# Kernel tuning notes

Hardware: AMD Instinct MI355X
Metric: run time of the kernel (lower is better)

## Reference

```python
import jax, jax.numpy as jnp
import numpy as np

SPARSITY = 0.5  # cur_sparsity set during training; 0.0 default would make masking a no-op
WEIGHT_BETA = 1.0
MASK_ALPHA1 = 1.0
MASK_ALPHA2 = 1.0


def binarize(mask_scores, sparsity):
    # SparseBinarizer.forward: prune (set to 0) the `num_prune` smallest scores globally.
    num_prune = int(mask_scores.size * sparsity)  # static: sparsity is a Python float
    flat = mask_scores.reshape(-1)
    prune_idx = jnp.argsort(flat)[:num_prune]
    mask = jnp.ones_like(flat).at[prune_idx].set(0.0)
    return mask.reshape(mask_scores.shape)


def setup_inputs() -> dict:
    key = jax.random.key(0)
    ks = jax.random.split(key, 9)
    out_f, in_f, r = 4096, 4096, 8
    tokens = 8192  # batch 4 * seq 2048
    return {
        "x": jax.random.normal(ks[0], (tokens, in_f), dtype=jnp.float32),
        "weight": jax.random.normal(ks[1], (out_f, in_f), dtype=jnp.float32) * 0.02,
        "bias": jax.random.normal(ks[2], (out_f,), dtype=jnp.float32) * 0.02,
        "weight_U": jax.random.normal(ks[3], (out_f, r), dtype=jnp.float32),
        "weight_V": jnp.zeros((r, in_f), dtype=jnp.float32),
        "mask_scores_A": jax.random.normal(ks[4], (out_f, r), dtype=jnp.float32),
        "mask_scores_B": jnp.zeros((r, in_f), dtype=jnp.float32),
        "mask_scores_R": jnp.zeros((out_f,), dtype=jnp.float32),
        "mask_scores_C": jnp.zeros((in_f,), dtype=jnp.float32),
    }


def reference(x, weight, bias, weight_U, weight_V, mask_scores_A, mask_scores_B,
              mask_scores_R, mask_scores_C):
    # weight = W + beta * U @ V   (low-rank weight reconstruction)
    w = weight + WEIGHT_BETA * (weight_U @ weight_V)
    # mask_scores = |w| + a1 * A @ B + a2 * (R[:,None] + C[None,:])
    mask_scores = (jnp.abs(w)
                   + MASK_ALPHA1 * (mask_scores_A @ mask_scores_B)
                   + MASK_ALPHA2 * (mask_scores_R[:, None] + mask_scores_C[None, :]))
    mask = binarize(mask_scores, SPARSITY)
    masked_weight = mask * w  # [out_f, in_f]
    # nn.Linear: x @ W^T + b
    return x @ masked_weight.T + bias
```

## Files before the change

kernel.cpp:

```cpp
#include <hip/hip_runtime.h>
#include <stdint.h>

#define TOKENS 8192
#define OUT_F  4096
#define IN_F   4096
#define RNK    8
#define KPRUNE 8388608u
#define CAP3   16384u

typedef unsigned short u16;
typedef float  f32x4  __attribute__((ext_vector_type(4)));
typedef short  bf16x8 __attribute__((ext_vector_type(8)));
typedef unsigned short u16x4 __attribute__((ext_vector_type(4)));
typedef unsigned short u16x8 __attribute__((ext_vector_type(8)));

#define XB_OFF    0ull
#define WB_OFF    67108864ull
#define CTL_OFF   100663296ull
#define H1_OFF    0
#define H2_OFF    16384
#define CNT3_OFF  32768
#define LIST3_OFF 32772
#define CTL_ZERO_U32 8193

__device__ __forceinline__ u16 f2bf(float f) {
    uint32_t u = __float_as_uint(f);
    u += 0x7fffu + ((u >> 16) & 1u);
    return (u16)(u >> 16);
}

__device__ __forceinline__ uint32_t fkey(float s) {
    uint32_t u = __float_as_uint(s);
    return (u & 0x80000000u) ? ~u : (u | 0x80000000u);
}

__device__ __forceinline__ void hsel(const uint32_t* __restrict__ hist, uint32_t k,
                                     volatile uint32_t* scr,
                                     uint32_t& bin, uint32_t& below)
{
    const int t = threadIdx.x;
    const int lane = t & 63, w = t >> 6;
    uint32_t v[16]; uint32_t s = 0;
#pragma unroll
    for (int j = 0; j < 16; ++j) { v[j] = hist[t*16 + j]; s += v[j]; }
    uint32_t sc = s;
#pragma unroll
    for (int d = 1; d < 64; d <<= 1) {
        uint32_t o = __shfl_up(sc, d, 64);
        if (lane >= d) sc += o;
    }
    if (lane == 63) scr[w] = sc;
    __syncthreads();
    uint32_t woff = 0;
    for (int ww = 0; ww < w; ++ww) woff += scr[ww];
    const uint32_t pre = woff + sc - s;
    if (pre < k && pre + s >= k) {
        uint32_t bb = pre;
#pragma unroll
        for (int j = 0; j < 16; ++j) {
            if (bb < k && bb + v[j] >= k) { scr[4] = (uint32_t)(t*16 + j); scr[5] = bb; }
            bb += v[j];
        }
    }
    __syncthreads();
    bin = scr[4]; below = scr[5];
    __syncthreads();
}

struct S2 { float4 w0, w1; uint4 k0, k1; };
__device__ __forceinline__ S2 score2(const float* __restrict__ W,
                                     const float* __restrict__ V,
                                     const float* __restrict__ B,
                                     const float* __restrict__ C,
                                     const float* uu0, const float* uu1,
                                     const float* aa0, const float* aa1,
                                     float ro0, float ro1, int o0, int i)
{
    const float4 cc = *(const float4*)&C[i];
    float4 w0 = *(const float4*)&W[(size_t)o0*IN_F + i];
    float4 w1 = *(const float4*)&W[(size_t)(o0+1)*IN_F + i];
#pragma unroll
    for (int r = 0; r < RNK; ++r) {
        const float4 v4 = *(const float4*)&V[r*IN_F + i];
        const float a0 = uu0[r], a1 = uu1[r];
        w0.x = fmaf(a0, v4.x, w0.x); w0.y = fmaf(a0, v4.y, w0.y);
        w0.z = fmaf(a0, v4.z, w0.z); w0.w = fmaf(a0, v4.w, w0.w);
        w1.x = fmaf(a1, v4.x, w1.x); w1.y = fmaf(a1, v4.y, w1.y);
        w1.z = fmaf(a1, v4.z, w1.z); w1.w = fmaf(a1, v4.w, w1.w);
    }
    float4 s0, s1;
    s0.x = fabsf(w0.x); s0.y = fabsf(w0.y); s0.z = fabsf(w0.z); s0.w = fabsf(w0.w);
    s1.x = fabsf(w1.x); s1.y = fabsf(w1.y); s1.z = fabsf(w1.z); s1.w = fabsf(w1.w);
#pragma unroll
    for (int r = 0; r < RNK; ++r) {
        const float4 b4 = *(const float4*)&B[r*IN_F + i];
        const float a0 = aa0[r], a1 = aa1[r];
        s0.x = fmaf(a0, b4.x, s0.x); s0.y = fmaf(a0, b4.y, s0.y);
        s0.z = fmaf(a0, b4.z, s0.z); s0.w = fmaf(a0, b4.w, s0.w);
        s1.x = fmaf(a1, b4.x, s1.x); s1.y = fmaf(a1, b4.y, s1.y);
        s1.z = fmaf(a1, b4.z, s1.z); s1.w = fmaf(a1, b4.w, s1.w);
    }
    s0.x += ro0 + cc.x; s0.y += ro0 + cc.y; s0.z += ro0 + cc.z; s0.w += ro0 + cc.w;
    s1.x += ro1 + cc.x; s1.y += ro1 + cc.y; s1.z += ro1 + cc.z; s1.w += ro1 + cc.w;
    S2 o;
    o.w0 = w0; o.w1 = w1;
    o.k0.x = fkey(s0.x); o.k0.y = fkey(s0.y); o.k0.z = fkey(s0.z); o.k0.w = fkey(s0.w);
    o.k1.x = fkey(s1.x); o.k1.y = fkey(s1.y); o.k1.z = fkey(s1.z); o.k1.w = fkey(s1.w);
    return o;
}

#define LOAD_ROWPARAMS                                                        \
    float uu0[RNK], uu1[RNK], aa0[RNK], aa1[RNK];                             \
    _Pragma("unroll") for (int r = 0; r < RNK; ++r) {                         \
        uu0[r] = U[o0*RNK + r];   uu1[r] = U[(o0+1)*RNK + r];                 \
        aa0[r] = A[o0*RNK + r];   aa1[r] = A[(o0+1)*RNK + r];                 \
    }                                                                         \
    const float ro0 = R[o0], ro1 = R[o0 + 1];

__global__ void convx_kernel(const float* __restrict__ x, u16* __restrict__ xB,
                             uint32_t* __restrict__ ctl)
{
    const int t = threadIdx.x;
    if (blockIdx.x < 33) {
        const int i = blockIdx.x * 256 + t;
        if (i < CTL_ZERO_U32) ctl[i] = 0u;
    }
    const size_t idx = (size_t)blockIdx.x * 256 + t;
    const float4* xv = (const float4*)x;
    float4 a = xv[idx*2];
    float4 b = xv[idx*2 + 1];
    u16x8 o;
    o[0]=f2bf(a.x); o[1]=f2bf(a.y); o[2]=f2bf(a.z); o[3]=f2bf(a.w);
    o[4]=f2bf(b.x); o[5]=f2bf(b.y); o[6]=f2bf(b.z); o[7]=f2bf(b.w);
    *((u16x8*)xB + idx) = o;
}

__global__ void prep_kernel(const float* __restrict__ W, const float* __restrict__ U,
                            const float* __restrict__ V, const float* __restrict__ A,
                            const float* __restrict__ B, const float* __restrict__ R,
                            const float* __restrict__ C, uint32_t* __restrict__ hist1)
{
    __shared__ uint32_t lh[4096];
    const int o0 = blockIdx.x * 2, t = threadIdx.x;
    for (int b = t; b < 4096; b += 256) lh[b] = 0u;
    LOAD_ROWPARAMS
    __syncthreads();
    for (int j = 0; j < IN_F/1024; ++j) {
        const int i = j*1024 + t*4;
        S2 s = score2(W, V, B, C, uu0, uu1, aa0, aa1, ro0, ro1, o0, i);
        atomicAdd(&lh[s.k0.x >> 20], 1u); atomicAdd(&lh[s.k0.y >> 20], 1u);
        atomicAdd(&lh[s.k0.z >> 20], 1u); atomicAdd(&lh[s.k0.w >> 20], 1u);
        atomicAdd(&lh[s.k1.x >> 20], 1u); atomicAdd(&lh[s.k1.y >> 20], 1u);
        atomicAdd(&lh[s.k1.z >> 20], 1u); atomicAdd(&lh[s.k1.w >> 20], 1u);
    }
    __syncthreads();
    for (int b = t; b < 4096; b += 256) { uint32_t c = lh[b]; if (c) atomicAdd(&hist1[b], c); }
}

__global__ void hist2r_kernel(const float* __restrict__ W, const float* __restrict__ U,
                              const float* __restrict__ V, const float* __restrict__ A,
                              const float* __restrict__ B, const float* __restrict__ R,
                              const float* __restrict__ C, const uint32_t* __restrict__ hist1,
                              uint32_t* __restrict__ hist2)
{
    __shared__ uint32_t lh[4096];
    __shared__ uint32_t scr[6];
    const int o0 = blockIdx.x * 2, t = threadIdx.x;
    uint32_t b1, below1;
    hsel(hist1, KPRUNE, scr, b1, below1);
    for (int b = t; b < 4096; b += 256) lh[b] = 0u;
    LOAD_ROWPARAMS
    __syncthreads();
    for (int j = 0; j < IN_F/1024; ++j) {
        const int i = j*1024 + t*4;
        S2 s = score2(W, V, B, C, uu0, uu1, aa0, aa1, ro0, ro1, o0, i);
        if ((s.k0.x >> 20) == b1) atomicAdd(&lh[(s.k0.x >> 8) & 0xFFFu], 1u);
        if ((s.k0.y >> 20) == b1) atomicAdd(&lh[(s.k0.y >> 8) & 0xFFFu], 1u);
        if ((s.k0.z >> 20) == b1) atomicAdd(&lh[(s.k0.z >> 8) & 0xFFFu], 1u);
        if ((s.k0.w >> 20) == b1) atomicAdd(&lh[(s.k0.w >> 8) & 0xFFFu], 1u);
        if ((s.k1.x >> 20) == b1) atomicAdd(&lh[(s.k1.x >> 8) & 0xFFFu], 1u);
        if ((s.k1.y >> 20) == b1) atomicAdd(&lh[(s.k1.y >> 8) & 0xFFFu], 1u);
        if ((s.k1.z >> 20) == b1) atomicAdd(&lh[(s.k1.z >> 8) & 0xFFFu], 1u);
        if ((s.k1.w >> 20) == b1) atomicAdd(&lh[(s.k1.w >> 8) & 0xFFFu], 1u);
    }
    __syncthreads();
    for (int b = t; b < 4096; b += 256) { uint32_t c = lh[b]; if (c) atomicAdd(&hist2[b], c); }
}

__global__ void applyr_kernel(const float* __restrict__ W, const float* __restrict__ U,
                              const float* __restrict__ V, const float* __restrict__ A,
                              const float* __restrict__ B, const float* __restrict__ R,
                              const float* __restrict__ C, const uint32_t* __restrict__ hist1,
                              const uint32_t* __restrict__ hist2, u16* __restrict__ wB,
                              uint32_t* __restrict__ cnt3, uint32_t* __restrict__ list3)
{
    __shared__ uint32_t scr[6];
    const int o0 = blockIdx.x * 2, t = threadIdx.x;
    uint32_t b1, below1, b2, below2;
    hsel(hist1, KPRUNE, scr, b1, below1);
    hsel(hist2, KPRUNE - below1, scr, b2, below2);
    const uint32_t pfx = (b1 << 12) | b2;
    LOAD_ROWPARAMS
    for (int j = 0; j < IN_F/1024; ++j) {
        const int i = j*1024 + t*4;
        S2 s = score2(W, V, B, C, uu0, uu1, aa0, aa1, ro0, ro1, o0, i);
        const float w0a[4] = {s.w0.x, s.w0.y, s.w0.z, s.w0.w};
        const float w1a[4] = {s.w1.x, s.w1.y, s.w1.z, s.w1.w};
        const uint32_t k0a[4] = {s.k0.x, s.k0.y, s.k0.z, s.k0.w};
        const uint32_t k1a[4] = {s.k1.x, s.k1.y, s.k1.z, s.k1.w};
        u16x4 b0, b1v;
#pragma unroll
        for (int e = 0; e < 4; ++e) {
            const uint32_t hi = k0a[e] >> 8;
            b0[e] = (hi < pfx) ? (u16)0 : f2bf(w0a[e]);
            if (hi == pfx) {
                uint32_t sl = atomicAdd(cnt3, 1u);
                if (sl < CAP3) list3[sl] = ((uint32_t)(o0*IN_F + i + e) << 8) | (k0a[e] & 0xFFu);
            }
        }
#pragma unroll
        for (int e = 0; e < 4; ++e) {
            const uint32_t hi = k1a[e] >> 8;
            b1v[e] = (hi < pfx) ? (u16)0 : f2bf(w1a[e]);
            if (hi == pfx) {
                uint32_t sl = atomicAdd(cnt3, 1u);
                if (sl < CAP3) list3[sl] = ((uint32_t)((o0+1)*IN_F + i + e) << 8) | (k1a[e] & 0xFFu);
            }
        }
        *(u16x4*)&wB[(size_t)o0*IN_F + i]     = b0;
        *(u16x4*)&wB[(size_t)(o0+1)*IN_F + i] = b1v;
    }
}

__global__ void selfix_kernel(const uint32_t* __restrict__ hist1, const uint32_t* __restrict__ hist2,
                              const uint32_t* __restrict__ cnt3, const uint32_t* __restrict__ list3,
                              u16* __restrict__ wB)
{
    __shared__ uint32_t lst[CAP3];
    __shared__ uint32_t lhist[256];
    __shared__ uint32_t sv[2];
    __shared__ uint32_t scr[6];
    const int t = threadIdx.x;
    uint32_t b1, below1, b2, below2;
    hsel(hist1, KPRUNE, scr, b1, below1);
    hsel(hist2, KPRUNE - below1, scr, b2, below2);
    const uint32_t k3 = KPRUNE - below1 - below2;
    uint32_t n = *cnt3; if (n > CAP3) n = CAP3;
    lhist[t] = 0u;
    __syncthreads();
    for (uint32_t i = t; i < n; i += 256) {
        const uint32_t e = list3[i];
        lst[i] = e;
        atomicAdd(&lhist[e & 0xFFu], 1u);
    }
    __syncthreads();
    uint32_t pre = 0;
    for (int b = 0; b < t; ++b) pre += lhist[b];
    if (pre < k3 && pre + lhist[t] >= k3) {
        sv[0] = (uint32_t)t;
        sv[1] = k3 - pre;
    }
    __syncthreads();
    const uint32_t b3 = sv[0], p = sv[1];
    for (uint32_t i = t; i < n; i += 256) {
        const uint32_t e = lst[i];
        const uint32_t lo = e & 0xFFu;
        if (lo < b3) { wB[e >> 8] = 0u; continue; }
        if (lo != b3) continue;
        uint32_t rank = 0;
        for (uint32_t j = 0; j < n; ++j) {
            const uint32_t f = lst[j];
            rank += ((f & 0xFFu) == b3 && f < e) ? 1u : 0u;
        }
        if (rank < p) wB[e >> 8] = 0u;
    }
}

#define A0H0   0
#define A0H1_0 16384
#define A0H1_1 32768
#define B0S    49152
#define A1H0   81920
#define A1H1_0 98304
#define A1H1_1 114688
#define B1S    131072

__device__ __forceinline__ void gl_lds16(const char* src, char* dst) {
    __builtin_amdgcn_global_load_lds((const __attribute__((address_space(1))) void*)src,
                                     (__attribute__((address_space(3))) void*)dst, 16, 0, 0);
}

__global__ __launch_bounds__(512, 2) void gemm256_kernel(const u16* __restrict__ xB,
                                                         const u16* __restrict__ wB,
                                                         const float* __restrict__ bias,
                                                         float* __restrict__ out)
{
    __shared__ char ldsc[163840];
    const int t    = threadIdx.x;
    const int lane = t & 63;
    const int wid  = t >> 6;
    const int wm   = wid >> 2;
    const int wn   = wid & 3;
    const int bid  = blockIdx.x;
    const int bn   = bid & 15;
    const int bm   = bid >> 4;

    const int l15 = lane & 15;
    const int kb  = (lane >> 4) << 4;
    const int rowA = 16*wm + l15;
    const int rowB = (wn & 1)*64 + l15;
    const int baseA = rowA*64 + (kb ^ (((rowA >> 1) & 3) << 4));
    const int baseB = rowB*64 + (kb ^ (((rowB >> 1) & 3) << 4));
    const char* aB0 = ldsc + baseA;
    const char* aB1 = ldsc + A1H0 + baseA;
    const char* bB0 = ldsc + B0S + (wn >> 1)*16384 + baseB;
    const char* bB1 = bB0 + (B1S - B0S);

    const int scol = ((t & 3) * 16) ^ (((t >> 3) & 3) << 4);
    const char* pA = (const char*)xB + ((size_t)(bm*256 + (t >> 2))) * (IN_F*2) + scol;
    const char* pB = (const char*)wB + ((size_t)(bn*256 + (t >> 2))) * (IN_F*2) + scol;
    const int tb16 = t * 16;

#define STAGEH(pG, slot, h, tile) do {                                        \
    const char* _s = (pG) + (size_t)(tile)*128 + (size_t)(h)*(128*IN_F*2);    \
    char* _d = ldsc + (slot) + tb16;                                          \
    gl_lds16(_s, _d);                                                         \
    gl_lds16(_s + 64, _d + 8192);                                             \
} while (0)

    f32x4  acc[8][4] = {};
    bf16x8 be[4][2], bo[4][2];
    bf16x8 au[2][2], av[2][2];

#define LOADBD(dst, bp) do {                                                  \
    _Pragma("unroll") for (int ni = 0; ni < 4; ++ni)                          \
    _Pragma("unroll") for (int kk = 0; kk < 2; ++kk)                          \
        dst[ni][kk] = *(const bf16x8*)((bp) + ni*1024 + kk*8192);             \
} while (0)

#define LOADAD(dst, ap, slot, q, mo) do {                                     \
    _Pragma("unroll") for (int mm = 0; mm < 2; ++mm)                          \
    _Pragma("unroll") for (int kk = 0; kk < 2; ++kk)                          \
        dst[mm][kk] = *(const bf16x8*)((ap) + (slot) +                        \
                      (2*(q)+mm-(mo))*2048 + kk*8192);                        \
} while (0)

#define MFMAQ(q, bb, aa) do {                                                 \
    _Pragma("unroll") for (int mm = 0; mm < 2; ++mm)                          \
    _Pragma("unroll") for (int ni = 0; ni < 4; ++ni)                          \
    _Pragma("unroll") for (int kk = 0; kk < 2; ++kk)                          \
        acc[2*(q)+mm][ni] = __builtin_amdgcn_mfma_f32_16x16x32_bf16(          \
            aa[mm][kk], bb[ni][kk], acc[2*(q)+mm][ni], 0, 0, 0);              \
} while (0)

#define PH_T(q, bb, aa, PRELOAD)                                              \
    __builtin_amdgcn_s_barrier();                                             \
    asm volatile("s_waitcnt lgkmcnt(0)" ::: "memory");                        \
    __builtin_amdgcn_s_setprio(1);                                            \
    MFMAQ(q, bb, aa);                                                         \
    PRELOAD;                                                                  \
    __builtin_amdgcn_s_setprio(0);                                            \
    __builtin_amdgcn_s_barrier();

#define STQ(q) do {                                                           \
    _Pragma("unroll") for (int mm = 0; mm < 2; ++mm) {                        \
        const int r0 = orow0 + 32*(2*(q)+mm);                                 \
        _Pragma("unroll") for (int ni = 0; ni < 4; ++ni) {                    \
            f32x4 v = acc[2*(q)+mm][ni];                                      \
            const int col = ocol0 + ni*16;                                    \
            _Pragma("unroll") for (int e = 0; e < 4; ++e)                     \
                out[(size_t)(r0 + e)*OUT_F + col] = v[e] + bv[ni];            \
        }                                                                     \
    }                                                                         \
} while (0)

#define PH_T_ST(q, bb, aa, PRELOAD)                                           \
    __builtin_amdgcn_s_barrier();                                             \
    asm volatile("s_waitcnt lgkmcnt(0)" ::: "memory");                        \
    __builtin_amdgcn_s_setprio(1);                                            \
    MFMAQ(q, bb, aa);                                                         \
    PRELOAD;                                                                  \
    __builtin_amdgcn_s_setprio(0);                                            \
    STQ(q);                                                                   \
    __builtin_amdgcn_s_barrier();

    STAGEH(pA, A0H1_0, 1, 0);
    STAGEH(pB, B0S,         0, 0);
    STAGEH(pB, B0S + 16384, 1, 0);
    STAGEH(pA, A0H0, 0, 0);
    STAGEH(pA, A1H1_0, 1, 1);
    STAGEH(pB, B1S,         0, 1);
    STAGEH(pB, B1S + 16384, 1, 1);
    STAGEH(pA, A1H0, 0, 1);
    asm volatile("s_waitcnt vmcnt(8)" ::: "memory");
    __builtin_amdgcn_s_barrier();
    LOADBD(be, bB0);
    LOADAD(au, aB0, A0H0, 0, 0);

#pragma unroll 1
    for (int j = 0; j < 31; ++j) {
        const int se = 2*j + 2;
        const int so = 2*j + 3;
        const int pc = j & 1;
        const int a0h1c = pc ? A0H1_1 : A0H1_0;
        const int a0h1n = pc ? A0H1_0 : A0H1_1;
        const int a1h1c = pc ? A1H1_1 : A1H1_0;
        const int a1h1n = pc ? A1H1_0 : A1H1_1;

        STAGEH(pA, a0h1n, 1, se);
        PH_T(0, be, au, LOADAD(av, aB0, A0H0, 1, 0))
        STAGEH(pB, B0S, 0, se);
        PH_T(1, be, av, LOADAD(au, aB0, a0h1c, 2, 4))
        STAGEH(pB, B0S + 16384, 1, se);
        PH_T(2, be, au, LOADAD(av, aB0, a0h1c, 3, 4))
        STAGEH(pA, A0H0, 0, se);
        asm volatile("s_waitcnt vmcnt(8)" ::: "memory");
        PH_T(3, be, av, { LOADBD(bo, bB1); LOADAD(au, aB1, 0, 0, 0); })

        STAGEH(pA, a1h1n, 1, so);
        PH_T(0, bo, au, LOADAD(av, aB1, 0, 1, 0))
        STAGEH(pB, B1S, 0, so);
        PH_T(1, bo, av, LOADAD(au, aB1, a1h1c - A1H0, 2, 4))
        STAGEH(pB, B1S + 16384, 1, so);
        PH_T(2, bo, au, LOADAD(av, aB1, a1h1c - A1H0, 3, 4))
        STAGEH(pA, A1H0, 0, so);
        asm volatile("s_waitcnt vmcnt(8)" ::: "memory");
        PH_T(3, bo, av, { LOADBD(be, bB0); LOADAD(au, aB0, A0H0, 0, 0); })
    }

    const int orow0 = bm*256 + 16*wm + ((lane >> 4) << 2);
    const int ocol0 = bn*256 + 64*wn + l15;
    float bv[4];
#pragma unroll
    for (int ni = 0; ni < 4; ++ni) bv[ni] = bias[ocol0 + ni*16];

    PH_T(0, be, au, LOADAD(av, aB0, A0H0, 1, 0))
    PH_T(1, be, av, LOADAD(au, aB0, A0H1_1, 2, 4))
    PH_T(2, be, au, LOADAD(av, aB0, A0H1_1, 3, 4))
    asm volatile("s_waitcnt vmcnt(0)" ::: "memory");
    PH_T(3, be, av, { LOADBD(bo, bB1); LOADAD(au, aB1, 0, 0, 0); })

    PH_T_ST(0, bo, au, LOADAD(av, aB1, 0, 1, 0))
    PH_T_ST(1, bo, av, LOADAD(au, aB1, A1H1_1 - A1H0, 2, 4))
    PH_T_ST(2, bo, au, LOADAD(av, aB1, A1H1_1 - A1H0, 3, 4))
    PH_T_ST(3, bo, av, (void)0)

#undef STAGEH
#undef LOADBD
#undef LOADAD
#undef MFMAQ
#undef PH_T
#undef PH_T_ST
#undef STQ
}

extern "C" void kernel_launch(void* const* d_in, const int* in_sizes, int n_in,
                              void* d_out, int out_size, void* d_ws, size_t ws_size,
                              hipStream_t stream)
{
    const float* x    = (const float*)d_in[0];
    const float* W    = (const float*)d_in[1];
    const float* bias = (const float*)d_in[2];
    const float* U    = (const float*)d_in[3];
    const float* V    = (const float*)d_in[4];
    const float* A    = (const float*)d_in[5];
    const float* B    = (const float*)d_in[6];
    const float* R    = (const float*)d_in[7];
    const float* C    = (const float*)d_in[8];
    float* out = (float*)d_out;

    char* ws = (char*)d_ws;
    u16*      xB    = (u16*)(ws + XB_OFF);
    u16*      wB    = (u16*)(ws + WB_OFF);
    uint32_t* ctl   = (uint32_t*)(ws + CTL_OFF);
    uint32_t* h1    = (uint32_t*)((char*)ctl + H1_OFF);
    uint32_t* h2    = (uint32_t*)((char*)ctl + H2_OFF);
    uint32_t* cnt3  = (uint32_t*)((char*)ctl + CNT3_OFF);
    uint32_t* list3 = (uint32_t*)((char*)ctl + LIST3_OFF);

    convx_kernel<<<TOKENS*IN_F/8/256, 256, 0, stream>>>(x, xB, ctl);
    prep_kernel<<<OUT_F/2, 256, 0, stream>>>(W, U, V, A, B, R, C, h1);
    hist2r_kernel<<<OUT_F/2, 256, 0, stream>>>(W, U, V, A, B, R, C, h1, h2);
    applyr_kernel<<<OUT_F/2, 256, 0, stream>>>(W, U, V, A, B, R, C, h1, h2, wB, cnt3, list3);
    selfix_kernel<<<1, 256, 0, stream>>>(h1, h2, cnt3, list3, wB);
    gemm256_kernel<<<(TOKENS/256)*(OUT_F/256), 512, 0, stream>>>(xB, wB, bias, out);
}
```

Baseline: 377.8 us.

## Restructure GEMM main loop to halve barriers and reorder global staging

Cuts the per-half-iteration barrier pairs in the bf16 MFMA main loop from eight phases to two barriers per half. MFMA quadrants are grouped in pairs, with LDS fragment loads interleaved between them. Global-to-LDS staging of the second buffer's A half is issued earlier, and the last vmcnt wait is relaxed to 6. This aims to lower barrier stalls and improve overlap, but it changes the hazard ordering between LDS writes and reads, which risks races and extra register pressure from holding both A fragments.

```diff
diff --git a/kernel.cpp b/kernel.cpp
--- a/kernel.cpp
+++ b/kernel.cpp
@@ -353,14 +353,10 @@
             aa[mm][kk], bb[ni][kk], acc[2*(q)+mm][ni], 0, 0, 0);              \
 } while (0)
 
-#define PH_T(q, bb, aa, PRELOAD)                                              \
-    __builtin_amdgcn_s_barrier();                                             \
-    asm volatile("s_waitcnt lgkmcnt(0)" ::: "memory");                        \
-    __builtin_amdgcn_s_setprio(1);                                            \
-    MFMAQ(q, bb, aa);                                                         \
-    PRELOAD;                                                                  \
-    __builtin_amdgcn_s_setprio(0);                                            \
-    __builtin_amdgcn_s_barrier();
+#define LGK0 asm volatile("s_waitcnt lgkmcnt(0)" ::: "memory");
+#define BAR  __builtin_amdgcn_s_barrier();
+#define PRIO1 __builtin_amdgcn_s_setprio(1);
+#define PRIO0 __builtin_amdgcn_s_setprio(0);
 
 #define STQ(q) do {                                                           \
     _Pragma("unroll") for (int mm = 0; mm < 2; ++mm) {                        \
@@ -374,16 +370,6 @@
     }                                                                         \
 } while (0)
 
-#define PH_T_ST(q, bb, aa, PRELOAD)                                           \
-    __builtin_amdgcn_s_barrier();                                             \
-    asm volatile("s_waitcnt lgkmcnt(0)" ::: "memory");                        \
-    __builtin_amdgcn_s_setprio(1);                                            \
-    MFMAQ(q, bb, aa);                                                         \
-    PRELOAD;                                                                  \
-    __builtin_amdgcn_s_setprio(0);                                            \
-    STQ(q);                                                                   \
-    __builtin_amdgcn_s_barrier();
-
     STAGEH(pA, A0H1_0, 1, 0);
     STAGEH(pB, B0S,         0, 0);
     STAGEH(pB, B0S + 16384, 1, 0);
@@ -393,9 +379,10 @@
     STAGEH(pB, B1S + 16384, 1, 1);
     STAGEH(pA, A1H0, 0, 1);
     asm volatile("s_waitcnt vmcnt(8)" ::: "memory");
-    __builtin_amdgcn_s_barrier();
+    BAR
     LOADBD(be, bB0);
     LOADAD(au, aB0, A0H0, 0, 0);
+    LOADAD(av, aB0, A0H0, 1, 0);
 
 #pragma unroll 1
     for (int j = 0; j < 31; ++j) {
@@ -408,24 +395,46 @@
         const int a1h1n = pc ? A1H1_0 : A1H1_1;
 
         STAGEH(pA, a0h1n, 1, se);
-        PH_T(0, be, au, LOADAD(av, aB0, A0H0, 1, 0))
-        STAGEH(pB, B0S, 0, se);
-        PH_T(1, be, av, LOADAD(au, aB0, a0h1c, 2, 4))
+        STAGEH(pA, a1h1n, 1, so);
+        LGK0 PRIO1
+        MFMAQ(0, be, au);
+        LOADAD(au, aB0, a0h1c, 2, 4);
+        MFMAQ(1, be, av);
+        LOADAD(av, aB0, a0h1c, 3, 4);
+        PRIO0 BAR
+
+        STAGEH(pB, B0S,         0, se);
         STAGEH(pB, B0S + 16384, 1, se);
-        PH_T(2, be, au, LOADAD(av, aB0, a0h1c, 3, 4))
+        LGK0 PRIO1
+        MFMAQ(2, be, au);
+        MFMAQ(3, be, av);
+        PRIO0
+        asm volatile("s_waitcnt vmcnt(8)" ::: "memory");
+        BAR
+        LOADBD(bo, bB1);
+        LOADAD(au, aB1, 0, 0, 0);
+        LOADAD(av, aB1, 0, 1, 0);
+
         STAGEH(pA, A0H0, 0, se);
-        asm volatile("s_waitcnt vmcnt(8)" ::: "memory");
-        PH_T(3, be, av, { LOADBD(bo, bB1); LOADAD(au, aB1, 0, 0, 0); })
-
-        STAGEH(pA, a1h1n, 1, so);
-        PH_T(0, bo, au, LOADAD(av, aB1, 0, 1, 0))
-        STAGEH(pB, B1S, 0, so);
-        PH_T(1, bo, av, LOADAD(au, aB1, a1h1c - A1H0, 2, 4))
+        LGK0 PRIO1
+        MFMAQ(0, bo, au);
+        LOADAD(au, aB1, a1h1c - A1H0, 2, 4);
+        MFMAQ(1, bo, av);
+        LOADAD(av, aB1, a1h1c - A1H0, 3, 4);
+        PRIO0 BAR
+
+        STAGEH(pB, B1S,         0, so);
         STAGEH(pB, B1S + 16384, 1, so);
-        PH_T(2, bo, au, LOADAD(av, aB1, a1h1c - A1H0, 3, 4))
         STAGEH(pA, A1H0, 0, so);
-        asm volatile("s_waitcnt vmcnt(8)" ::: "memory");
-        PH_T(3, bo, av, { LOADBD(be, bB0); LOADAD(au, aB0, A0H0, 0, 0); })
+        LGK0 PRIO1
+        MFMAQ(2, bo, au);
+        MFMAQ(3, bo, av);
+        PRIO0
+        asm volatile("s_waitcnt vmcnt(6)" ::: "memory");
+        BAR
+        LOADBD(be, bB0);
+        LOADAD(au, aB0, A0H0, 0, 0);
+        LOADAD(av, aB0, A0H0, 1, 0);
     }
 
     const int orow0 = bm*256 + 16*wm + ((lane >> 4) << 2);
@@ -434,23 +443,43 @@
 #pragma unroll
     for (int ni = 0; ni < 4; ++ni) bv[ni] = bias[ocol0 + ni*16];
 
-    PH_T(0, be, au, LOADAD(av, aB0, A0H0, 1, 0))
-    PH_T(1, be, av, LOADAD(au, aB0, A0H1_1, 2, 4))
-    PH_T(2, be, au, LOADAD(av, aB0, A0H1_1, 3, 4))
+    LGK0 PRIO1
+    MFMAQ(0, be, au);
+    LOADAD(au, aB0, A0H1_1, 2, 4);
+    MFMAQ(1, be, av);
+    LOADAD(av, aB0, A0H1_1, 3, 4);
+    PRIO0
+    LGK0 PRIO1
+    MFMAQ(2, be, au);
+    MFMAQ(3, be, av);
+    PRIO0
     asm volatile("s_waitcnt vmcnt(0)" ::: "memory");
-    PH_T(3, be, av, { LOADBD(bo, bB1); LOADAD(au, aB1, 0, 0, 0); })
-
-    PH_T_ST(0, bo, au, LOADAD(av, aB1, 0, 1, 0))
-    PH_T_ST(1, bo, av, LOADAD(au, aB1, A1H1_1 - A1H0, 2, 4))
-    PH_T_ST(2, bo, au, LOADAD(av, aB1, A1H1_1 - A1H0, 3, 4))
-    PH_T_ST(3, bo, av, (void)0)
+    BAR
+    LOADBD(bo, bB1);
+    LOADAD(au, aB1, 0, 0, 0);
+    LOADAD(av, aB1, 0, 1, 0);
+
+    LGK0 PRIO1
+    MFMAQ(0, bo, au);
+    LOADAD(au, aB1, A1H1_1 - A1H0, 2, 4);
+    MFMAQ(1, bo, av);
+    LOADAD(av, aB1, A1H1_1 - A1H0, 3, 4);
+    PRIO0
+    STQ(0); STQ(1);
+    LGK0 PRIO1
+    MFMAQ(2, bo, au);
+    MFMAQ(3, bo, av);
+    PRIO0
+    STQ(2); STQ(3);
 
 #undef STAGEH
 #undef LOADBD
 #undef LOADAD
 #undef MFMAQ
-#undef PH_T
-#undef PH_T_ST
+#undef LGK0
+#undef BAR
+#undef PRIO1
+#undef PRIO0
 #undef STQ
 }
 
```

Measured after the change: 382.6 us. Within noise of the previous version (+1.3%).
